# Performance work log

Hardware: AMD Instinct MI355X
Metric: run time of the kernel (lower is better)

Reference implementation:

```python
import jax, jax.numpy as jnp
import numpy as np

DISPS = (8, 8, 4, 2)
STRIDES = (2, 1, 1, 1)
DG = 4      # deformable groups
PAD = 1     # (kernel_size-1)//2 for k=3
KH = KW = 3


def pointwise_corr(f1, f2, disp, stride):
    """Windowed pointwise cross-correlation.
    f1, f2: [B, C, H, W]. Returns [B, (2d+1)^2, H, W], dy-major shift order,
    displacement step = stride, normalized by channel count.
    """
    B, C, H, W = f1.shape
    pad = disp * stride
    f2p = jnp.pad(f2, ((0, 0), (0, 0), (pad, pad), (pad, pad)))
    rng = np.arange(2 * disp + 1) * stride
    shifts = np.stack(np.meshgrid(rng, rng, indexing='ij'), -1).reshape(-1, 2)
    shifts = jnp.asarray(shifts, jnp.int32)

    def one(s):
        f2s = jax.lax.dynamic_slice(f2p, (0, 0, s[0], s[1]), (B, C, H, W))
        return jnp.sum(f1 * f2s, axis=1) / C   # [B, H, W]

    corr = jax.vmap(one)(shifts)               # [K2, B, H, W]
    return jnp.transpose(corr, (1, 0, 2, 3))


def bilinear_sample(img, y, x):
    """img: [cg, H, W]; y, x: [K2, H, W] float sample coords.
    Zero outside boundaries (deform-conv semantics). Returns [cg, K2, H, W]."""
    cg, H, W = img.shape
    y0 = jnp.floor(y); x0 = jnp.floor(x)
    wy = y - y0;       wx = x - x0
    y0i = y0.astype(jnp.int32); x0i = x0.astype(jnp.int32)

    def gather(iy, ix):
        valid = (iy >= 0) & (iy < H) & (ix >= 0) & (ix < W)
        v = img[:, jnp.clip(iy, 0, H - 1), jnp.clip(ix, 0, W - 1)]  # [cg,K2,H,W]
        return v * valid.astype(img.dtype)

    v00 = gather(y0i,     x0i)
    v01 = gather(y0i,     x0i + 1)
    v10 = gather(y0i + 1, x0i)
    v11 = gather(y0i + 1, x0i + 1)
    return (v00 * (1 - wy) * (1 - wx) + v01 * (1 - wy) * wx
            + v10 * wy * (1 - wx) + v11 * wy * wx)


def deform_conv(x, offset, weight, dg, pad):
    """Deformable conv v1, stride 1. x: [N,C,H,W]; offset: [N, dg*2*K2, H, W]
    (per group, per kernel point, (dy,dx)); weight: [O, C, kh, kw]."""
    N, C, H, W = x.shape
    O, _, kh, kw = weight.shape
    K2 = kh * kw
    cg = C // dg
    off = offset.reshape(N, dg, K2, 2, H, W)
    ky, kx = np.meshgrid(np.arange(kh), np.arange(kw), indexing='ij')
    ky = jnp.asarray(ky.reshape(-1), jnp.float32)
    kx = jnp.asarray(kx.reshape(-1), jnp.float32)
    gy = jnp.arange(H, dtype=jnp.float32)
    gx = jnp.arange(W, dtype=jnp.float32)
    base_y = ky[:, None, None] - pad + gy[None, :, None]   # [K2,H,1]
    base_x = kx[:, None, None] - pad + gx[None, None, :]   # [K2,1,W]
    ys = base_y[None, None] + off[:, :, :, 0]              # [N,dg,K2,H,W]
    xs = base_x[None, None] + off[:, :, :, 1]
    xg = x.reshape(N, dg, cg, H, W)
    sampled = jax.vmap(jax.vmap(bilinear_sample))(xg, ys, xs)  # [N,dg,cg,K2,H,W]
    w = weight.reshape(O, dg, cg, K2)
    return jnp.einsum('ogck,ngckhw->nohw', w, sampled)


def _forward_single(x, w_off, w_adapt, disp, stride):
    T, B, C, H, W = x.shape
    corrs = [pointwise_corr(x[t], x[t - 1], disp, stride) for t in range(1, T)]
    corr = jnp.concatenate(corrs, axis=0)                   # [(T-1)*B, K2, H, W]
    offset = jnp.einsum('ok,bkhw->bohw', w_off, corr)       # 1x1 conv, no bias
    feat_in = x[1:].reshape((T - 1) * B, C, H, W)
    feat = jax.nn.relu(deform_conv(feat_in, offset, w_adapt, DG, PAD))
    return jnp.concatenate([x[0], feat], axis=0)            # [T*B, C, H, W]


def setup_inputs() -> dict:
    key = jax.random.key(0)
    ks = jax.random.split(key, 12)
    shapes = [(2, 2, 256, 64, 64), (2, 2, 256, 32, 32),
              (2, 2, 256, 16, 16), (2, 2, 256, 8, 8)]
    d = {}
    for i, s in enumerate(shapes):
        d[f"x{i}"] = jax.random.normal(ks[i], s, jnp.float32)
    for i, disp in enumerate(DISPS):
        K2 = (2 * disp + 1) ** 2
        d[f"w_off{i}"] = 0.01 * jax.random.normal(ks[4 + i], (DG * 2 * KH * KW, K2), jnp.float32)
        d[f"w_adapt{i}"] = 0.01 * jax.random.normal(ks[8 + i], (256, 256, KH, KW), jnp.float32)
    return d


def reference(x0, x1, x2, x3, w_off0, w_off1, w_off2, w_off3,
              w_adapt0, w_adapt1, w_adapt2, w_adapt3):
    xs = [x0, x1, x2, x3]
    w_offs = [w_off0, w_off1, w_off2, w_off3]
    w_adapts = [w_adapt0, w_adapt1, w_adapt2, w_adapt3]
    outs = [_forward_single(xs[l], w_offs[l], w_adapts[l], DISPS[l], STRIDES[l])
            for l in range(4)]
    return tuple(outs)
```

## Files before the change

kernel.cpp:

```cpp
#include <hip/hip_runtime.h>

typedef unsigned int u32;
typedef unsigned short u16;
typedef _Float16 f16x2 __attribute__((ext_vector_type(2)));
typedef _Float16 f16x8 __attribute__((ext_vector_type(8)));
typedef __bf16 bf16x8 __attribute__((ext_vector_type(8)));
typedef float f32x4 __attribute__((ext_vector_type(4)));

static __device__ __forceinline__ f16x2 bch(u32 u) { return __builtin_bit_cast(f16x2, u); }


__global__ __launch_bounds__(256) void prep_kernel(
    const float* __restrict__ x0, const float* __restrict__ x1,
    const float* __restrict__ x2, const float* __restrict__ x3,
    const float* __restrict__ w0, const float* __restrict__ w1,
    const float* __restrict__ w2, const float* __restrict__ w3,
    u32* __restrict__ xq, u16* __restrict__ A, float* __restrict__ offs,
    float* __restrict__ out)
{
  __shared__ u32 plds[32 * 65];
  int bx = blockIdx.x, t = threadIdx.x;
  if (bx < 3060) {
    int i = bx * 256 + t;
    if (i < 783360) offs[i] = 0.f;
    return;
  }
  if (bx < 4420) {
    int local = bx - 3060;
    const float* xs; int lvlb, lgW, lgnch;
    if (local < 1024)      { xs = x0; lvlb = 0;       lgW = 6; lgnch = 6; }
    else if (local < 1280) { xs = x1; lvlb = 2097152; lgW = 5; lgnch = 4; local -= 1024; }
    else if (local < 1344) { xs = x2; lvlb = 2621440; lgW = 4; lgnch = 2; local -= 1280; }
    else                   { xs = x3; lvlb = 2752512; lgW = 3; lgnch = 0; local -= 1344; }
    int HW = 1 << (2 * lgW);
    int hc = local & ((1 << lgnch) - 1);
    int g  = (local >> lgnch) & 3;
    int tb = local >> (lgnch + 2);
    int hw0 = hc * 64;
    int lane = t & 63, qd = t >> 6;
#pragma unroll
    for (int j = 0; j < 8; ++j) {
      int cpw = qd * 8 + j;
      int c = tb * 256 + g * 64 + cpw * 2;
      const float* s = xs + (size_t)c * HW + hw0 + lane;
      float f0 = s[0], f1 = s[HW];
      f16x2 h; h[0] = (_Float16)f0; h[1] = (_Float16)f1;
      plds[cpw * 65 + lane] = __builtin_bit_cast(u32, h);
    }
    __syncthreads();
    u32* dst = xq + lvlb + (size_t)(tb * 4 + g) * HW * 32 + (size_t)hw0 * 32;
#pragma unroll
    for (int j = 0; j < 8; ++j) {
      int ow = j * 256 + t;
      int hwl = ow >> 5, ww = ow & 31;
      dst[(size_t)hwl * 32 + ww] = plds[ww * 65 + hwl];
    }
    return;
  }
  if (bx < 13636) {
    int i = (bx - 4420) * 256 + t;
    if (i >= 2359296) return;
    int lv = i / 589824;
    const float* w = (lv == 0) ? w0 : (lv == 1) ? w1 : (lv == 2) ? w2 : w3;
    int local = i - lv * 589824;
    int o = local / 2304;
    int k = local - o * 2304;
    int g = k / 576;
    int r = k - g * 576;
    int p = r >> 6;
    int c = r & 63;
    float v = w[(size_t)(o * 256 + g * 64 + c) * 9 + p];
    __bf16 bv = (__bf16)v;
    A[i] = __builtin_bit_cast(u16, bv);
    return;
  }
  {
    int i = (bx - 13636) * 256 + t;
    const float* xs; int base, dstb;
    if (i < 2097152)      { xs = x0; base = 0;       dstb = 0; }
    else if (i < 2621440) { xs = x1; base = 2097152; dstb = 4194304; }
    else if (i < 2752512) { xs = x2; base = 2621440; dstb = 5242880; }
    else if (i < 2785280) { xs = x3; base = 2752512; dstb = 5505024; }
    else return;
    int local = i - base;
    out[(size_t)dstb + local] = xs[local];
  }
}

__global__ __launch_bounds__(256) void corr_mfma_kernel(const u32* __restrict__ xq, float* __restrict__ corr)
{
  __shared__ __align__(16) u32 lds[8192];
  int t = threadIdx.x, bx = blockIdx.x;

  if (bx >= 1472) {
    int gw = ((bx - 1472) * 256 + t) >> 6;
    int lane = t & 63;
    int cs = lane >> 4, hwi = lane & 15;
    int obase = gw * 16;
    int K2, R, DISP, lgW, xqlb, crb, rel;
    if (obase < 41472)      { K2 = 81; R = 9; DISP = 4; lgW = 4; xqlb = 2621440; crb = 2959360; rel = obase; }
    else if (obase < 44672) { K2 = 25; R = 5; DISP = 2; lgW = 3; xqlb = 2752512; crb = 3000832; rel = obase - 41472; }
    else return;
    int W = 1 << lgW, HW = W * W;
    int hw = (rel & (HW - 1)) + hwi;
    int rr = rel >> (2 * lgW);
    int k = rr % K2, b = rr / K2;
    int h = hw >> lgW, wc = hw & (W - 1);
    int dy = k / R - DISP, dx = k % R - DISP;
    int h2 = h + dy, w2 = wc + dx;
    float a = 0.f;
    if ((u32)h2 < (u32)W && (u32)w2 < (u32)W) {
      const u32* q1 = xq + xqlb + ((size_t)((2 + b) * 4 + cs) * HW + hw) * 32;
      const u32* q0 = xq + xqlb + ((size_t)(b * 4 + cs) * HW + (h2 * W + w2)) * 32;
#pragma unroll 8
      for (int j = 0; j < 32; ++j)
        a = __builtin_amdgcn_fdot2(bch(q1[j]), bch(q0[j]), a, false);
    }
    a += __shfl_xor(a, 16);
    a += __shfl_xor(a, 32);
    if (cs == 0) corr[crb + rel + hwi] = a * 0.00390625f;
    return;
  }

  int l = t & 63, w = t >> 6;
  int lvl, b, y, kq, lgW, W, HW, xqlb, crb;
  if (bx < 1152) { lvl = 0; int r = bx;        kq = r % 9; r /= 9; y = r & 63; b = r >> 6;
                   lgW = 6; W = 64; HW = 4096; xqlb = 0;       crb = 0; }
  else           { lvl = 1; int r = bx - 1152; kq = r % 5; r /= 5; y = r & 31; b = r >> 5;
                   lgW = 5; W = 32; HW = 1024; xqlb = 2097152; crb = 2367488; }
  int par, qy, storeok;
  if (lvl == 0) { int rr = w >> 1; par = w & 1; qy = (kq < 8) ? 2 * kq + rr : 16;
                  storeok = !(kq == 8 && w >= 2); }
  else          { par = 0; qy = 4 * kq + w; storeok = (qy <= 16); if (qy > 16) qy = 16; }
  int rowY = (lvl == 0) ? (y + 2 * qy - 16) : (y + qy - 8);
  int f1words = (lvl == 0) ? 1024 : 512;
  int tb1 = 2 + b, tb0 = b;

  bool f1do = (lvl == 0) || (w < 2);
  u32 f1_lo; int f1_dw;
  {
    int G = w * 64 + l;
    int px = G >> 2, s = G & 3;
    int i = px & 31;
    int pari = px >> 5;
    int x = (lvl == 0) ? (2 * i + pari) : px;
    int cg = (s ^ ((i & 3) ^ ((i >> 2) & 3))) & 3;
    f1_lo = (u32)(xqlb + (y * W + x) * 32 + cg * 4);
    f1_dw = w * 256;
  }
  u32 f2_lo[3], f2_mask[3]; int f2_dw[3];
#pragma unroll
  for (int q = 0; q < 3; ++q) {
    int F = q * 64 + l;
    int jp = F >> 2, s = F & 3;
    int cg = (s ^ ((jp & 3) ^ ((jp >> 2) & 3))) & 3;
    int xs = (lvl == 0) ? (2 * (jp - 8) + par) : (jp - 8);
    bool valid = ((u32)xs < (u32)W) && ((u32)rowY < (u32)W);
    f2_lo[q]   = valid ? (u32)(xqlb + (rowY * W + xs) * 32 + cg * 4) : 6968960u;
    f2_mask[q] = valid ? 0xFFFFFFFFu : 0u;
    f2_dw[q]   = f1words + w * 768 + q * 256;
  }
  int lr = l & 15, lk = l >> 4;
  int aoff[2], boff[3];
#pragma unroll
  for (int it = 0; it < 2; ++it) {
    int iA = it * 16 + lr;
    int px = ((lvl == 0) ? par * 32 : 0) + iA;
    int phys = (lk ^ ((iA & 3) ^ ((iA >> 2) & 3))) & 3;
    aoff[it] = (px * 16 + phys * 4) * 4;
  }
#pragma unroll
  for (int T = 0; T < 3; ++T) {
    int jp = T * 16 + lr;
    int phys = (lk ^ ((jp & 3) ^ ((jp >> 2) & 3))) & 3;
    boff[T] = (f1words + w * 768 + jp * 16 + phys * 4) * 4;
  }

  f32x4 acc0 = {0,0,0,0}, acc1 = {0,0,0,0}, acc2 = {0,0,0,0}, acc3 = {0,0,0,0};

  auto issue = [&](int ch, int sel) {
    int g2 = ch >> 1, hf = ch & 1;
    u32 cb1 = ((u32)(tb1 * 4 + g2) * (u32)HW) * 32u + (u32)hf * 16u;
    u32 cb0 = ((u32)(tb0 * 4 + g2) * (u32)HW) * 32u + (u32)hf * 16u;
    u32* lb = &lds[sel * 4096];
    if (f1do)
      __builtin_amdgcn_global_load_lds(xq + cb1 + f1_lo, lb + f1_dw, 16, 0, 0);
#pragma unroll
    for (int q = 0; q < 3; ++q)
      __builtin_amdgcn_global_load_lds(xq + ((cb0 & f2_mask[q]) + f2_lo[q]), lb + f2_dw[q], 16, 0, 0);
  };

  issue(0, 0);
#pragma unroll 1
  for (int ch = 0; ch < 8; ++ch) {
    int sel = ch & 1;
    asm volatile("s_waitcnt vmcnt(0)" ::: "memory");
    asm volatile("s_barrier" ::: "memory");
    __builtin_amdgcn_sched_barrier(0);
    if (ch < 7) issue(ch + 1, sel ^ 1);
    const char* lb = (const char*)&lds[sel * 4096];
    f16x8 A0 = *(const f16x8*)(lb + aoff[0]);
    f16x8 A1 = *(const f16x8*)(lb + aoff[1]);
    f16x8 B0 = *(const f16x8*)(lb + boff[0]);
    f16x8 B1 = *(const f16x8*)(lb + boff[1]);
    f16x8 B2 = *(const f16x8*)(lb + boff[2]);
    acc0 = __builtin_amdgcn_mfma_f32_16x16x32_f16(A0, B0, acc0, 0, 0, 0);
    acc1 = __builtin_amdgcn_mfma_f32_16x16x32_f16(A0, B1, acc1, 0, 0, 0);
    acc2 = __builtin_amdgcn_mfma_f32_16x16x32_f16(A1, B1, acc2, 0, 0, 0);
    acc3 = __builtin_amdgcn_mfma_f32_16x16x32_f16(A1, B2, acc3, 0, 0, 0);
  }

  if (!storeok) return;
  const float sc = 0.00390625f;
#pragma unroll
  for (int tile = 0; tile < 4; ++tile) {
    int it = (tile >= 2) ? 1 : 0;
    int T  = (tile == 0) ? 0 : (tile == 3) ? 2 : 1;
    f32x4 av = (tile == 0) ? acc0 : (tile == 1) ? acc1 : (tile == 2) ? acc2 : acc3;
    int jp = T * 16 + lr;
#pragma unroll
    for (int jj = 0; jj < 4; ++jj) {
      int i = it * 16 + lk * 4 + jj;
      int qx = jp - i;
      if (qx >= 0 && qx <= 16) {
        int xo = (lvl == 0) ? (2 * i + par) : i;
        int k = qy * 17 + qx;
        corr[crb + (size_t)(b * 289 + k) * HW + y * W + xo] = av[jj] * sc;
      }
    }
  }
}

__global__ __launch_bounds__(256) void offset_kernel(
    const float* __restrict__ corr,
    const float* __restrict__ wo0, const float* __restrict__ wo1,
    const float* __restrict__ wo2, const float* __restrict__ wo3,
    float* __restrict__ offs)
{
  int t = threadIdx.x, bx = blockIdx.x;
  int kc = bx % 6;
  int unit = bx / 6;
  int og = unit & 3;
  int pb = unit >> 2;

  int lgW, K2, crb, ofb, pbl;
  const float* wo;
  if (pb < 32)      { pbl = pb;      lgW = 6; K2 = 289; crb = 0;       ofb = 0;      wo = wo0; }
  else if (pb < 40) { pbl = pb - 32; lgW = 5; K2 = 289; crb = 2367488; ofb = 589824; wo = wo1; }
  else if (pb < 42) { pbl = pb - 40; lgW = 4; K2 = 81;  crb = 2959360; ofb = 737280; wo = wo2; }
  else              { pbl = 0;       lgW = 3; K2 = 25;  crb = 3000832; ofb = 774144; wo = wo3; }
  int HW = 1 << (2 * lgW);
  int pxg = pbl * 256 + t;
  if (lgW == 3 && t >= 128) return;
  int b = pxg >> (2 * lgW);
  int hw = pxg & (HW - 1);

  int kchunk = (K2 + 5) / 6;
  int klo = kc * kchunk;
  int khi = klo + kchunk; if (khi > K2) khi = K2;
  if (klo >= khi) return;

  const float* cr = corr + crb + (size_t)b * K2 * HW + hw;
  const float* wp = wo + (size_t)og * 18 * K2;
  float acc[18];
#pragma unroll
  for (int j = 0; j < 18; ++j) acc[j] = 0.f;
#pragma unroll 2
  for (int k = klo; k < khi; ++k) {
    float cv = cr[(size_t)k * HW];
#pragma unroll
    for (int j = 0; j < 18; ++j) acc[j] = fmaf(wp[(size_t)j * K2 + k], cv, acc[j]);
  }
  float* op = offs + ofb + ((size_t)b * 72 + og * 18) * HW + hw;
#pragma unroll
  for (int j = 0; j < 18; ++j) atomicAdd(&op[(size_t)j * HW], acc[j]);
}

__global__ __launch_bounds__(256) void sample_kernel(
    const u32* __restrict__ xq, const float* __restrict__ offs,
    u16* __restrict__ Bbuf, int Rg0, int nrows)
{
  int tid = blockIdx.x * 256 + threadIdx.x;
  if (tid >= nrows * 144) return;
  int r_l = tid / 144;
  int rem = tid - r_l * 144;
  int gp = rem >> 2, cq = rem & 3;
  int Rg = Rg0 + r_l;
  int b, hw, lgW, xqlb, ofb;
  if (Rg < 8192)       { b = Rg >> 12;       hw = Rg & 4095;  lgW = 6; xqlb = 0;       ofb = 0; }
  else if (Rg < 10240) { int r = Rg - 8192;  b = r >> 10; hw = r & 1023; lgW = 5; xqlb = 2097152; ofb = 589824; }
  else if (Rg < 10752) { int r = Rg - 10240; b = r >> 8;  hw = r & 255;  lgW = 4; xqlb = 2621440; ofb = 737280; }
  else                 { int r = Rg - 10752; b = r >> 6;  hw = r & 63;   lgW = 3; xqlb = 2752512; ofb = 774144; }
  int W = 1 << lgW, HW = W * W;
  u16* rowp = Bbuf + (size_t)r_l * 2304;

  size_t ob = (size_t)ofb + ((size_t)b * 72 + gp * 2) * HW + hw;
  float ody = offs[ob], odx = offs[ob + HW];
  int g = gp / 9, p = gp - g * 9;
  int ky = p / 3, kx = p - ky * 3;
  int sh = hw >> lgW, sw = hw & (W - 1);
  float ys = (float)(sh + ky - 1) + ody;
  float xs = (float)(sw + kx - 1) + odx;
  float y0f = floorf(ys), x0f = floorf(xs);
  float wy = ys - y0f, wx = xs - x0f;
  int y0 = (int)y0f, x0 = (int)x0f, y1 = y0 + 1, x1 = x0 + 1;
  bool vy0 = (u32)y0 < (u32)W, vy1 = (u32)y1 < (u32)W;
  bool vx0 = (u32)x0 < (u32)W, vx1 = (u32)x1 < (u32)W;
  float w00 = (1.f - wy) * (1.f - wx), w01 = (1.f - wy) * wx;
  float w10 = wy * (1.f - wx), w11 = wy * wx;
  const u32* base = xq + xqlb + ((size_t)((2 + b) * 4 + g) * HW) * 32 + cq * 8;
  const uint4 z = make_uint4(0, 0, 0, 0);
  uint4 a00 = z, c00 = z, a01 = z, c01 = z, a10 = z, c10 = z, a11 = z, c11 = z;
  if (vy0 && vx0) { const u32* p0 = base + (size_t)(y0 * W + x0) * 32; a00 = *(const uint4*)p0; c00 = *(const uint4*)(p0 + 4); }
  if (vy0 && vx1) { const u32* p0 = base + (size_t)(y0 * W + x1) * 32; a01 = *(const uint4*)p0; c01 = *(const uint4*)(p0 + 4); }
  if (vy1 && vx0) { const u32* p0 = base + (size_t)(y1 * W + x0) * 32; a10 = *(const uint4*)p0; c10 = *(const uint4*)(p0 + 4); }
  if (vy1 && vx1) { const u32* p0 = base + (size_t)(y1 * W + x1) * 32; a11 = *(const uint4*)p0; c11 = *(const uint4*)(p0 + 4); }
  bf16x8 r0, r1;
#pragma unroll
  for (int ww = 0; ww < 4; ++ww) {
    f16x2 h00 = bch(((const u32*)&a00)[ww]);
    f16x2 h01 = bch(((const u32*)&a01)[ww]);
    f16x2 h10 = bch(((const u32*)&a10)[ww]);
    f16x2 h11 = bch(((const u32*)&a11)[ww]);
    float lo = w00 * (float)h00[0] + w01 * (float)h01[0] + w10 * (float)h10[0] + w11 * (float)h11[0];
    float hi = w00 * (float)h00[1] + w01 * (float)h01[1] + w10 * (float)h10[1] + w11 * (float)h11[1];
    r0[2 * ww] = (__bf16)lo; r0[2 * ww + 1] = (__bf16)hi;
  }
#pragma unroll
  for (int ww = 0; ww < 4; ++ww) {
    f16x2 h00 = bch(((const u32*)&c00)[ww]);
    f16x2 h01 = bch(((const u32*)&c01)[ww]);
    f16x2 h10 = bch(((const u32*)&c10)[ww]);
    f16x2 h11 = bch(((const u32*)&c11)[ww]);
    float lo = w00 * (float)h00[0] + w01 * (float)h01[0] + w10 * (float)h10[0] + w11 * (float)h11[0];
    float hi = w00 * (float)h00[1] + w01 * (float)h01[1] + w10 * (float)h10[1] + w11 * (float)h11[1];
    r1[2 * ww] = (__bf16)lo; r1[2 * ww + 1] = (__bf16)hi;
  }
  u16* dst = rowp + gp * 64 + cq * 16;
  *(bf16x8*)dst = r0;
  *(bf16x8*)(dst + 8) = r1;
}

__global__ __launch_bounds__(256) void gemm2_kernel(
    const u16* __restrict__ A, const u16* __restrict__ Bbuf,
    int Rg0, float* __restrict__ out)
{
  __shared__ __align__(16) u16 Al[2][64 * 72];
  __shared__ __align__(16) u16 Bl[2][64 * 72];
  int t = threadIdx.x, bx = blockIdx.x;
  int mt = bx & 3, nt = bx >> 2;
  int Rgt = Rg0 + nt * 64;
  int b, hw0, lgW, Ab, outb;
  if (Rgt < 8192)       { b = Rgt >> 12;       hw0 = Rgt & 4095;  lgW = 6; Ab = 0;       outb = 2097152; }
  else if (Rgt < 10240) { int r = Rgt - 8192;  b = r >> 10; hw0 = r & 1023; lgW = 5; Ab = 589824;  outb = 4718592; }
  else if (Rgt < 10752) { int r = Rgt - 10240; b = r >> 8;  hw0 = r & 255;  lgW = 4; Ab = 1179648; outb = 5373952; }
  else                  { int r = Rgt - 10752; b = r >> 6;  hw0 = r & 63;   lgW = 3; Ab = 1769472; outb = 5537792; }
  int HW = 1 << (2 * lgW);
  const u16* Bbase = Bbuf + (size_t)(Rgt - Rg0) * 2304;

  int o0 = mt * 64;
  int l = t & 63, wv = t >> 6;
  int lr = l & 15, lk = l >> 4;
  int wvr = wv >> 1, wvc = wv & 1;

  int srow = t >> 2, sc4 = t & 3;
  const u16* Asrc = A + Ab + (size_t)(o0 + srow) * 2304 + sc4 * 16;
  const u16* Bsrc = Bbase + (size_t)srow * 2304 + sc4 * 16;

  f32x4 acc[2][2];
#pragma unroll
  for (int i = 0; i < 2; ++i)
#pragma unroll
    for (int j = 0; j < 2; ++j) acc[i][j] = (f32x4){0, 0, 0, 0};

  uint4 pa0, pa1, pb0, pb1;
  auto issue = [&](int kt) {
    const uint4* as = (const uint4*)(Asrc + kt * 64);
    const uint4* bs = (const uint4*)(Bsrc + kt * 64);
    pa0 = as[0]; pa1 = as[1];
    pb0 = bs[0]; pb1 = bs[1];
  };
  auto commit = [&](int sel) {
    *(uint4*)(&Al[sel][srow * 72 + sc4 * 16]) = pa0;
    *(uint4*)(&Al[sel][srow * 72 + sc4 * 16 + 8]) = pa1;
    *(uint4*)(&Bl[sel][srow * 72 + sc4 * 16]) = pb0;
    *(uint4*)(&Bl[sel][srow * 72 + sc4 * 16 + 8]) = pb1;
  };

  issue(0); commit(0);
  issue(1);
  __syncthreads();
#pragma unroll 1
  for (int kt = 0; kt < 36; ++kt) {
    int sel = kt & 1;
#pragma unroll
    for (int kk = 0; kk < 2; ++kk) {
      bf16x8 b0 = *(const bf16x8*)(&Bl[sel][(wvc * 32 + lr) * 72 + kk * 32 + lk * 8]);
      bf16x8 b1 = *(const bf16x8*)(&Bl[sel][(wvc * 32 + 16 + lr) * 72 + kk * 32 + lk * 8]);
      bf16x8 a0 = *(const bf16x8*)(&Al[sel][(wvr * 32 + lr) * 72 + kk * 32 + lk * 8]);
      bf16x8 a1 = *(const bf16x8*)(&Al[sel][(wvr * 32 + 16 + lr) * 72 + kk * 32 + lk * 8]);
      acc[0][0] = __builtin_amdgcn_mfma_f32_16x16x32_bf16(a0, b0, acc[0][0], 0, 0, 0);
      acc[0][1] = __builtin_amdgcn_mfma_f32_16x16x32_bf16(a0, b1, acc[0][1], 0, 0, 0);
      acc[1][0] = __builtin_amdgcn_mfma_f32_16x16x32_bf16(a1, b0, acc[1][0], 0, 0, 0);
      acc[1][1] = __builtin_amdgcn_mfma_f32_16x16x32_bf16(a1, b1, acc[1][1], 0, 0, 0);
    }
    if (kt < 35) commit(sel ^ 1);
    __syncthreads();
    if (kt < 34) issue(kt + 2);
  }

  float* op = out + outb + (size_t)b * 256 * HW;
#pragma unroll
  for (int ar = 0; ar < 2; ++ar)
#pragma unroll
    for (int bc = 0; bc < 2; ++bc)
#pragma unroll
      for (int j = 0; j < 4; ++j) {
        int orow = o0 + wvr * 32 + ar * 16 + lk * 4 + j;
        int col = hw0 + wvc * 32 + bc * 16 + lr;
        op[(size_t)orow * HW + col] = fmaxf(acc[ar][bc][j], 0.f);
      }
}

extern "C" void kernel_launch(void* const* d_in, const int* in_sizes, int n_in,
                              void* d_out, int out_size, void* d_ws, size_t ws_size,
                              hipStream_t stream) {
  const float* x[4];
  const float* woff[4];
  const float* wad[4];
  for (int l = 0; l < 4; ++l) {
    x[l]    = (const float*)d_in[l];
    woff[l] = (const float*)d_in[4 + 2 * l];
    wad[l]  = (const float*)d_in[5 + 2 * l];
  }
  float* out = (float*)d_out;
  char* ws = (char*)d_ws;
  u32*   xq   = (u32*)(ws);
  u16*   A    = (u16*)(ws + 11141120);
  float* corr = (float*)(ws + 15859712);
  float* offs = (float*)(ws + 27875840);
  u16* BbufS = (u16*)(ws + 15859712);
  u16* BbufL = (u16*)(ws + 31009280);
  int big = (ws_size >= (size_t)81144320) ? 1 : 0;

  prep_kernel<<<24516, 256, 0, stream>>>(x[0], x[1], x[2], x[3],
                                         wad[0], wad[1], wad[2], wad[3], xq, A, offs, out);
  corr_mfma_kernel<<<2170, 256, 0, stream>>>(xq, corr);
  offset_kernel<<<1032, 256, 0, stream>>>(corr, woff[0], woff[1], woff[2], woff[3], offs);

  if (big) {
    sample_kernel<<<6120, 256, 0, stream>>>(xq, offs, BbufL, 0, 10880);
    gemm2_kernel<<<680, 256, 0, stream>>>(A, BbufL, 0, out);
  } else {
    for (int ph = 0; ph < 5; ++ph) {
      int Rg0 = ph * 2560;
      int nrows = (ph < 4) ? 2560 : 640;
      int sgrid = (nrows * 144 + 255) / 256;
      int ggrid = (nrows / 64) * 4;
      sample_kernel<<<sgrid, 256, 0, stream>>>(xq, offs, BbufS, Rg0, nrows);
      gemm2_kernel<<<ggrid, 256, 0, stream>>>(A, BbufS, Rg0, out);
    }
  }
}
```

Baseline: 132.1 us.

## Deepen gemm2 global prefetch to two stages and swizzle block order

Restructures the gemm2 main loop to unroll by two with two register prefetch sets, so global loads are issued two k-tiles ahead instead of one. This hides more global memory latency behind the MFMA work. It also remaps block indices with a stride-8 swizzle so neighbouring blocks touch different N tiles. The cost is more live registers, which may lower occupancy, and a different L2 access pattern.

```diff
diff --git a/kernel.cpp b/kernel.cpp
--- a/kernel.cpp
+++ b/kernel.cpp
@@ -341,6 +341,25 @@
   *(bf16x8*)(dst + 8) = r1;
 }
 
+#define G_ISSUE(P, kt) { const uint4* as_ = (const uint4*)(Asrc + (kt) * 64); \
+                         const uint4* bs_ = (const uint4*)(Bsrc + (kt) * 64); \
+                         a0##P = as_[0]; a1##P = as_[1]; b0##P = bs_[0]; b1##P = bs_[1]; }
+#define G_COMMIT(P, sel) { *(uint4*)(&Al[sel][srow * 72 + sc4 * 16]) = a0##P; \
+                           *(uint4*)(&Al[sel][srow * 72 + sc4 * 16 + 8]) = a1##P; \
+                           *(uint4*)(&Bl[sel][srow * 72 + sc4 * 16]) = b0##P; \
+                           *(uint4*)(&Bl[sel][srow * 72 + sc4 * 16 + 8]) = b1##P; }
+#define G_MFMA(sel) { _Pragma("unroll") \
+  for (int kk = 0; kk < 2; ++kk) { \
+    bf16x8 fb0 = *(const bf16x8*)(&Bl[sel][(wvc * 32 + lr) * 72 + kk * 32 + lk * 8]); \
+    bf16x8 fb1 = *(const bf16x8*)(&Bl[sel][(wvc * 32 + 16 + lr) * 72 + kk * 32 + lk * 8]); \
+    bf16x8 fa0 = *(const bf16x8*)(&Al[sel][(wvr * 32 + lr) * 72 + kk * 32 + lk * 8]); \
+    bf16x8 fa1 = *(const bf16x8*)(&Al[sel][(wvr * 32 + 16 + lr) * 72 + kk * 32 + lk * 8]); \
+    acc[0][0] = __builtin_amdgcn_mfma_f32_16x16x32_bf16(fa0, fb0, acc[0][0], 0, 0, 0); \
+    acc[0][1] = __builtin_amdgcn_mfma_f32_16x16x32_bf16(fa0, fb1, acc[0][1], 0, 0, 0); \
+    acc[1][0] = __builtin_amdgcn_mfma_f32_16x16x32_bf16(fa1, fb0, acc[1][0], 0, 0, 0); \
+    acc[1][1] = __builtin_amdgcn_mfma_f32_16x16x32_bf16(fa1, fb1, acc[1][1], 0, 0, 0); \
+  } }
+
 __global__ __launch_bounds__(256) void gemm2_kernel(
     const u16* __restrict__ A, const u16* __restrict__ Bbuf,
     int Rg0, float* __restrict__ out)
@@ -348,7 +367,9 @@
   __shared__ __align__(16) u16 Al[2][64 * 72];
   __shared__ __align__(16) u16 Bl[2][64 * 72];
   int t = threadIdx.x, bx = blockIdx.x;
-  int mt = bx & 3, nt = bx >> 2;
+  int nb = gridDim.x;
+  int gsw = (bx & 7) * (nb >> 3) + (bx >> 3);
+  int mt = gsw & 3, nt = gsw >> 2;
   int Rgt = Rg0 + nt * 64;
   int b, hw0, lgW, Ab, outb;
   if (Rgt < 8192)       { b = Rgt >> 12;       hw0 = Rgt & 4095;  lgW = 6; Ab = 0;       outb = 2097152; }
@@ -373,40 +394,23 @@
 #pragma unroll
     for (int j = 0; j < 2; ++j) acc[i][j] = (f32x4){0, 0, 0, 0};
 
-  uint4 pa0, pa1, pb0, pb1;
-  auto issue = [&](int kt) {
-    const uint4* as = (const uint4*)(Asrc + kt * 64);
-    const uint4* bs = (const uint4*)(Bsrc + kt * 64);
-    pa0 = as[0]; pa1 = as[1];
-    pb0 = bs[0]; pb1 = bs[1];
-  };
-  auto commit = [&](int sel) {
-    *(uint4*)(&Al[sel][srow * 72 + sc4 * 16]) = pa0;
-    *(uint4*)(&Al[sel][srow * 72 + sc4 * 16 + 8]) = pa1;
-    *(uint4*)(&Bl[sel][srow * 72 + sc4 * 16]) = pb0;
-    *(uint4*)(&Bl[sel][srow * 72 + sc4 * 16 + 8]) = pb1;
-  };
-
-  issue(0); commit(0);
-  issue(1);
+  uint4 a0A, a1A, b0A, b1A, a0B, a1B, b0B, b1B;
+
+  G_ISSUE(A, 0); G_COMMIT(A, 0);
+  G_ISSUE(B, 1);
+  G_ISSUE(A, 2);
   __syncthreads();
 #pragma unroll 1
-  for (int kt = 0; kt < 36; ++kt) {
-    int sel = kt & 1;
-#pragma unroll
-    for (int kk = 0; kk < 2; ++kk) {
-      bf16x8 b0 = *(const bf16x8*)(&Bl[sel][(wvc * 32 + lr) * 72 + kk * 32 + lk * 8]);
-      bf16x8 b1 = *(const bf16x8*)(&Bl[sel][(wvc * 32 + 16 + lr) * 72 + kk * 32 + lk * 8]);
-      bf16x8 a0 = *(const bf16x8*)(&Al[sel][(wvr * 32 + lr) * 72 + kk * 32 + lk * 8]);
-      bf16x8 a1 = *(const bf16x8*)(&Al[sel][(wvr * 32 + 16 + lr) * 72 + kk * 32 + lk * 8]);
-      acc[0][0] = __builtin_amdgcn_mfma_f32_16x16x32_bf16(a0, b0, acc[0][0], 0, 0, 0);
-      acc[0][1] = __builtin_amdgcn_mfma_f32_16x16x32_bf16(a0, b1, acc[0][1], 0, 0, 0);
-      acc[1][0] = __builtin_amdgcn_mfma_f32_16x16x32_bf16(a1, b0, acc[1][0], 0, 0, 0);
-      acc[1][1] = __builtin_amdgcn_mfma_f32_16x16x32_bf16(a1, b1, acc[1][1], 0, 0, 0);
-    }
-    if (kt < 35) commit(sel ^ 1);
+  for (int k2 = 0; k2 < 18; ++k2) {
+    int kt = 2 * k2;
+    G_MFMA(0);
+    if (kt < 35) G_COMMIT(B, 1);
     __syncthreads();
-    if (kt < 34) issue(kt + 2);
+    if (kt + 3 < 36) G_ISSUE(B, kt + 3);
+    G_MFMA(1);
+    if (kt + 1 < 35) G_COMMIT(A, 0);
+    __syncthreads();
+    if (kt + 4 < 36) G_ISSUE(A, kt + 4);
   }
 
   float* op = out + outb + (size_t)b * 256 * HW;
```

New measurement: 127.9 us. 3.2% less time.
